# Kernel tuning notes

Hardware: AMD Instinct MI355X
Metric: run time of the kernel (lower is better)

Reference implementation:

```python
import jax, jax.numpy as jnp
import numpy as np

# token_type_vocab constants (closed over; original passes a dict)
WORD_TOKEN, SMILES_TOKEN, VALUE_TOKEN, CLS_TOKEN, SEP_TOKEN, MASK_TOKEN = 0, 1, 2, 3, 4, 5
FP_DIM, HID, COL_VOCAB, MAX_POS, TT_VOCAB = 768, 768, 1000, 512, 8
B, S = 64, 512


def setup_inputs() -> dict:
    key = jax.random.key(0)
    ks = jax.random.split(key, 16)
    scale = 0.02
    return {
        "batch_size": B,
        "max_batch_seq_len": S,
        "SMILES_fps": jax.random.normal(ks[0], (B, S, FP_DIM), jnp.float32),
        "word_tokens_ref": jax.random.randint(ks[1], (B, S), 0, COL_VOCAB),
        "values_ref": jax.random.normal(ks[2], (B, S), jnp.float32),
        "token_type_ids": jax.random.randint(ks[3], (B, S), 0, 6),
        "position_ids": jax.random.randint(ks[4], (B, S), 0, MAX_POS),
        "fc1_w": jax.random.normal(ks[5], (FP_DIM, 4 * FP_DIM), jnp.float32) * scale,
        "fc1_b": jnp.zeros((4 * FP_DIM,), jnp.float32),
        "fc2_w": jax.random.normal(ks[6], (4 * FP_DIM, HID), jnp.float32) * scale,
        "fc2_b": jnp.zeros((HID,), jnp.float32),
        "prop_emb": jax.random.normal(ks[7], (COL_VOCAB, HID), jnp.float32) * scale,
        "val_w": jax.random.normal(ks[8], (HID,), jnp.float32) * scale,  # Linear(1, HID) weight
        "val_b": jnp.zeros((HID,), jnp.float32),
        "pos_emb": jax.random.normal(ks[9], (MAX_POS, HID), jnp.float32) * scale,
        "type_emb": jax.random.normal(ks[10], (TT_VOCAB, HID), jnp.float32) * scale,
        "ln_g": jnp.ones((HID,), jnp.float32),
        "ln_b": jnp.zeros((HID,), jnp.float32),
    }


def reference(batch_size, max_batch_seq_len, SMILES_fps, word_tokens_ref, values_ref,
              token_type_ids, position_ids, fc1_w, fc1_b, fc2_w, fc2_b, prop_emb,
              val_w, val_b, pos_emb, type_emb, ln_g, ln_b):
    word_mask = token_type_ids == WORD_TOKEN
    smiles_mask = token_type_ids == SMILES_TOKEN
    value_mask = token_type_ids == VALUE_TOKEN
    # Faithful to source: '&' of mutually exclusive equalities -> always False
    special_mask = (token_type_ids == CLS_TOKEN) & (token_type_ids == SEP_TOKEN) & (token_type_ids == MASK_TOKEN)

    # branch embeddings computed densely, selected per token (masks are disjoint)
    word_e = prop_emb[word_tokens_ref]                                   # [B,S,H]
    smiles_e = jax.nn.relu(jnp.einsum('bsf,fd->bsd', SMILES_fps, fc1_w) + fc1_b)
    smiles_e = jnp.einsum('bsf,fd->bsd', smiles_e, fc2_w) + fc2_b        # [B,S,H]
    value_e = values_ref[..., None] * val_w + val_b                      # [B,S,H]
    special_e = type_emb[token_type_ids]                                 # [B,S,H]

    input_embeddings = jnp.zeros_like(word_e)
    input_embeddings = jnp.where(word_mask[..., None], word_e, input_embeddings)
    input_embeddings = jnp.where(smiles_mask[..., None], smiles_e, input_embeddings)
    input_embeddings = jnp.where(value_mask[..., None], value_e, input_embeddings)
    input_embeddings = jnp.where(special_mask[..., None], special_e, input_embeddings)

    emb = input_embeddings + pos_emb[position_ids] + type_emb[token_type_ids]
    mu = jnp.mean(emb, axis=-1, keepdims=True)
    var = jnp.mean(jnp.square(emb - mu), axis=-1, keepdims=True)
    emb = (emb - mu) * jax.lax.rsqrt(var + 1e-12) * ln_g + ln_b
    return emb  # dropout_rate=0 (eval): identity
```

## Files before the change

### kernel.cpp

```cpp
#include <hip/hip_runtime.h>
#include <hip/hip_bf16.h>
#include <stdint.h>


typedef __bf16 bf16x8 __attribute__((ext_vector_type(8)));
typedef float f32x4 __attribute__((ext_vector_type(4)));

__device__ __forceinline__ unsigned short f2bf(float f) {
  union { float f; unsigned int u; } c; c.f = f;
  unsigned int u = c.u;
  return (unsigned short)((u + 0x7FFFu + ((u >> 16) & 1u)) >> 16);
}
__device__ __forceinline__ float bf2f(unsigned short b) {
  union { unsigned int u; float f; } c; c.u = ((unsigned int)b) << 16;
  return c.f;
}
__device__ __forceinline__ void barrier_sync() {
  asm volatile("" ::: "memory");
  __builtin_amdgcn_sched_barrier(0);
  __builtin_amdgcn_s_barrier();
  __builtin_amdgcn_sched_barrier(0);
  asm volatile("" ::: "memory");
}

__global__ __launch_bounds__(256) void k_prep(
    const float* __restrict__ fc1_w, const float* __restrict__ fc2_w,
    unsigned short* __restrict__ w1t, unsigned short* __restrict__ w2t,
    int* __restrict__ counter) {
  if (blockIdx.x == 0 && threadIdx.x == 0) *counter = 0;
  __shared__ float tile[32][33];
  int b = blockIdx.x;
  const float* src;
  unsigned short* dst;
  int R, C, bx, by;
  if (b < 2304) {
    src = fc1_w; dst = w1t; R = 768; C = 3072;
    bx = (b % 96) * 32; by = (b / 96) * 32;
  } else {
    b -= 2304;
    src = fc2_w; dst = w2t; R = 3072; C = 768;
    bx = (b % 24) * 32; by = (b / 24) * 32;
  }
  int tx = threadIdx.x & 31;
  int ty = threadIdx.x >> 5;
#pragma unroll
  for (int i = 0; i < 4; i++) {
    int r = by + ty + i * 8;
    tile[ty + i * 8][tx] = src[(size_t)r * C + bx + tx];
  }
  __syncthreads();
#pragma unroll
  for (int i = 0; i < 4; i++) {
    int c = bx + ty + i * 8;
    dst[(size_t)c * R + by + tx] = f2bf(tile[tx][ty + i * 8]);
  }
}

__global__ void k_compact(const int* __restrict__ tt, int* __restrict__ counter,
                          int* __restrict__ idx, int* __restrict__ slot, int BS) {
  int t = blockIdx.x * 256 + threadIdx.x;
  if (t >= BS) return;
  if (tt[t] == 1) {
    int s = atomicAdd(counter, 1);
    idx[s] = t;
    slot[t] = s;
  }
}

__global__ __launch_bounds__(256) void k_gather(
    const float* __restrict__ fps, const int* __restrict__ idx,
    const int* __restrict__ counter, unsigned short* __restrict__ A1, int cap) {
  int wave = threadIdx.x >> 6, lane = threadIdx.x & 63;
  int s = blockIdx.x * 4 + wave;
  int n = *counter;
  int n_pad = (n + 127) & ~127;
  if (n_pad > cap) n_pad = cap;
  if (s >= n_pad) return;
  ushort4* dst = (ushort4*)(A1 + (size_t)s * 768);
  if (s < n) {
    const float4* srcr = (const float4*)(fps + (size_t)idx[s] * 768);
#pragma unroll
    for (int i = 0; i < 3; i++) {
      float4 v = srcr[lane + (i << 6)];
      ushort4 o;
      o.x = f2bf(v.x); o.y = f2bf(v.y); o.z = f2bf(v.z); o.w = f2bf(v.w);
      dst[lane + (i << 6)] = o;
    }
  } else {
    ushort4 z = {0, 0, 0, 0};
#pragma unroll
    for (int i = 0; i < 3; i++) dst[lane + (i << 6)] = z;
  }
}

template <int MODE, int NB, int KS, int AST, int BST>
__global__ __launch_bounds__(256) void k_gemm(
    const unsigned short* __restrict__ A,
    const unsigned short* __restrict__ BT,
    const float* __restrict__ bias,
    unsigned short* __restrict__ C,
    const int* __restrict__ counter, int N, int cap) {
  int n = *counter;
  int n_pad = (n + 127) & ~127;
  if (n_pad > cap) n_pad = cap;
  const int mb = n_pad >> 7;

  constexpr int NCOL = NB * KS;
  constexpr int C_CH = (KS > 1) ? ((KS == 4) ? 4 : 2) : 2;
  constexpr int A_CH = 8 / C_CH;
  constexpr int CLEN = NCOL / C_CH;
  constexpr int KSL = AST / KS;
  constexpr int KITER = KSL / 64;

  const int bid = blockIdx.x;
  const int xcd = bid & 7;
  const int j = bid >> 3;
  const int mc = xcd / C_CH, cc = xcd % C_CH;
  const int q = mb / A_CH, r = mb % A_CH;
  const int mlen = q + (mc < r ? 1 : 0);
  const int mbase = mc * q + (mc < r ? mc : r);
  if (j >= mlen * CLEN) return;
  const int m_blk = mbase + j / CLEN;
  const int c_blk = cc * CLEN + j % CLEN;
  const int ks = c_blk / NB;
  const int nb = c_blk % NB;
  const int m0 = m_blk * 128, n0 = nb * 128;
  const int k0g = ks * KSL;

  __shared__ __attribute__((aligned(128))) char smem[65536];
  auto lds = (__attribute__((address_space(3))) char*)smem;

  const int t = threadIdx.x;
  const int wave = t >> 6;
  const int lane = t & 63;
  const int wm = (wave >> 1) * 64;
  const int wn = (wave & 1) * 64;

  f32x4 acc[4][4] = {};

  auto stage = [&](int kt, int bufbase) {
#pragma unroll
    for (int i = 0; i < 4; i++) {
      int c = i * 256 + t;
      int rr = c >> 3;
      int k8 = ((c & 7) ^ (rr & 7)) << 3;
      const unsigned short* ga = A + (size_t)(m0 + rr) * AST + k0g + kt * 64 + k8;
      __builtin_amdgcn_global_load_lds(
          (const __attribute__((address_space(1))) void*)ga,
          (__attribute__((address_space(3))) void*)(lds + bufbase + i * 4096 + wave * 1024),
          16, 0, 0);
    }
#pragma unroll
    for (int i = 0; i < 4; i++) {
      int c = i * 256 + t;
      int rr = c >> 3;
      int k8 = ((c & 7) ^ (rr & 7)) << 3;
      const unsigned short* gb = BT + (size_t)(n0 + rr) * BST + k0g + kt * 64 + k8;
      __builtin_amdgcn_global_load_lds(
          (const __attribute__((address_space(1))) void*)gb,
          (__attribute__((address_space(3))) void*)(lds + bufbase + 16384 + i * 4096 + wave * 1024),
          16, 0, 0);
    }
  };

  stage(0, 0);
  for (int it = 0; it < KITER; ++it) {
    const int cur = it & 1, nxt = cur ^ 1;
    if (it + 1 < KITER) {
      stage(it + 1, nxt * 32768);
      __builtin_amdgcn_sched_barrier(0);
      asm volatile("s_waitcnt vmcnt(8)" ::: "memory");
    } else {
      asm volatile("s_waitcnt vmcnt(0)" ::: "memory");
    }
    barrier_sync();
    const int bufbase = cur * 32768;
#pragma unroll
    for (int kk = 0; kk < 2; kk++) {
      bf16x8 af[4], bfr[4];
      int kbyte = (kk * 32 + ((lane >> 4) * 8)) * 2;
#pragma unroll
      for (int mi = 0; mi < 4; mi++) {
        int rr = wm + mi * 16 + (lane & 15);
        af[mi] = *(const bf16x8*)(smem + bufbase + rr * 128 + (kbyte ^ ((rr & 7) << 4)));
      }
#pragma unroll
      for (int ni = 0; ni < 4; ni++) {
        int rr = wn + ni * 16 + (lane & 15);
        bfr[ni] = *(const bf16x8*)(smem + bufbase + 16384 + rr * 128 + (kbyte ^ ((rr & 7) << 4)));
      }
#pragma unroll
      for (int mi = 0; mi < 4; mi++)
#pragma unroll
        for (int ni = 0; ni < 4; ni++)
          acc[mi][ni] = __builtin_amdgcn_mfma_f32_16x16x32_bf16(
              af[mi], bfr[ni], acc[mi][ni], 0, 0, 0);
    }
    asm volatile("s_waitcnt lgkmcnt(0)" ::: "memory");
    barrier_sync();
  }

#pragma unroll
  for (int ni = 0; ni < 4; ni++) {
    int col = n0 + wn + ni * 16 + (lane & 15);
    float bv = (MODE == 1) ? bias[col] : 0.f;
#pragma unroll
    for (int mi = 0; mi < 4; mi++) {
#pragma unroll
      for (int j2 = 0; j2 < 4; j2++) {
        int row = m0 + wm + mi * 16 + ((lane >> 4) * 4) + j2;
        float v = acc[mi][ni][j2] + bv;
        if constexpr (MODE == 1) {
          v = v > 0.f ? v : 0.f;
          C[(size_t)row * N + col] = f2bf(v);
        } else {
          C[((size_t)ks * cap + row) * N + col] = f2bf(v);
        }
      }
    }
  }
}

__global__ __launch_bounds__(256) void k_assemble(
    const unsigned short* __restrict__ sout, const float* __restrict__ fc2b,
    const int* __restrict__ slot,
    const int* __restrict__ ttid, const int* __restrict__ word,
    const float* __restrict__ values, const int* __restrict__ posid,
    const float* __restrict__ prop, const float* __restrict__ valw,
    const float* __restrict__ valb, const float* __restrict__ pose,
    const float* __restrict__ tye, const float* __restrict__ lng,
    const float* __restrict__ lnb, float* __restrict__ out, int BS, int cap) {
  int wave = threadIdx.x >> 6, lane = threadIdx.x & 63;
  int t = blockIdx.x * 4 + wave;
  if (t >= BS) return;
  int tt = ttid[t];

  float v[12];
  if (tt == 1) {
    int sl = slot[t];
    const ushort4* pr[2];
#pragma unroll
    for (int p = 0; p < 2; p++)
      pr[p] = (const ushort4*)(sout + ((size_t)p * cap + sl) * 768);
    const float4* b4 = (const float4*)fc2b;
#pragma unroll
    for (int i = 0; i < 3; i++) {
      float4 b = b4[lane + (i << 6)];
      float a0 = b.x, a1 = b.y, a2 = b.z, a3 = b.w;
#pragma unroll
      for (int p = 0; p < 2; p++) {
        ushort4 u = pr[p][lane + (i << 6)];
        a0 += bf2f(u.x); a1 += bf2f(u.y); a2 += bf2f(u.z); a3 += bf2f(u.w);
      }
      v[4 * i] = a0; v[4 * i + 1] = a1; v[4 * i + 2] = a2; v[4 * i + 3] = a3;
    }
  } else if (tt == 0) {
    const float4* row = (const float4*)(prop + (size_t)word[t] * 768);
#pragma unroll
    for (int i = 0; i < 3; i++) {
      float4 x = row[lane + (i << 6)];
      v[4 * i] = x.x; v[4 * i + 1] = x.y; v[4 * i + 2] = x.z; v[4 * i + 3] = x.w;
    }
  } else if (tt == 2) {
    float val = values[t];
#pragma unroll
    for (int i = 0; i < 3; i++) {
      float4 w = ((const float4*)valw)[lane + (i << 6)];
      float4 b = ((const float4*)valb)[lane + (i << 6)];
      v[4 * i] = val * w.x + b.x; v[4 * i + 1] = val * w.y + b.y;
      v[4 * i + 2] = val * w.z + b.z; v[4 * i + 3] = val * w.w + b.w;
    }
  } else {
#pragma unroll
    for (int j = 0; j < 12; j++) v[j] = 0.f;
  }

  const float4* p4 = (const float4*)(pose + (size_t)posid[t] * 768);
  const float4* ty4 = (const float4*)(tye + (size_t)tt * 768);
#pragma unroll
  for (int i = 0; i < 3; i++) {
    float4 p = p4[lane + (i << 6)];
    float4 y = ty4[lane + (i << 6)];
    v[4 * i] += p.x + y.x; v[4 * i + 1] += p.y + y.y;
    v[4 * i + 2] += p.z + y.z; v[4 * i + 3] += p.w + y.w;
  }

  float s = 0.f;
#pragma unroll
  for (int j = 0; j < 12; j++) s += v[j];
#pragma unroll
  for (int o = 32; o >= 1; o >>= 1) s += __shfl_xor(s, o);
  float mu = s * (1.0f / 768.0f);

  float qv = 0.f;
#pragma unroll
  for (int j = 0; j < 12; j++) { float d = v[j] - mu; qv += d * d; }
#pragma unroll
  for (int o = 32; o >= 1; o >>= 1) qv += __shfl_xor(qv, o);
  float rs = 1.0f / sqrtf(qv * (1.0f / 768.0f) + 1e-12f);

  float4* o4 = (float4*)(out + (size_t)t * 768);
#pragma unroll
  for (int i = 0; i < 3; i++) {
    float4 g = ((const float4*)lng)[lane + (i << 6)];
    float4 b = ((const float4*)lnb)[lane + (i << 6)];
    float4 r;
    r.x = (v[4 * i] - mu) * rs * g.x + b.x;
    r.y = (v[4 * i + 1] - mu) * rs * g.y + b.y;
    r.z = (v[4 * i + 2] - mu) * rs * g.z + b.z;
    r.w = (v[4 * i + 3] - mu) * rs * g.w + b.w;
    o4[lane + (i << 6)] = r;
  }
}

extern "C" void kernel_launch(void* const* d_in, const int* in_sizes, int n_in,
                              void* d_out, int out_size, void* d_ws, size_t ws_size,
                              hipStream_t stream) {
  const int BS = in_sizes[3];
  const float* fps    = (const float*)d_in[2];
  const int*   word   = (const int*)d_in[3];
  const float* values = (const float*)d_in[4];
  const int*   tt     = (const int*)d_in[5];
  const int*   pos    = (const int*)d_in[6];
  const float* fc1_w  = (const float*)d_in[7];
  const float* fc1_b  = (const float*)d_in[8];
  const float* fc2_w  = (const float*)d_in[9];
  const float* fc2_b  = (const float*)d_in[10];
  const float* prop   = (const float*)d_in[11];
  const float* valw   = (const float*)d_in[12];
  const float* valb   = (const float*)d_in[13];
  const float* pose   = (const float*)d_in[14];
  const float* tye    = (const float*)d_in[15];
  const float* lng    = (const float*)d_in[16];
  const float* lnb    = (const float*)d_in[17];
  float* out = (float*)d_out;

  char* ws = (char*)d_ws;
  const size_t off_idx  = 256;
  const size_t off_slot = off_idx + (size_t)BS * 4;
  const size_t off_w1t  = off_slot + (size_t)BS * 4;
  const size_t off_w2t  = off_w1t + (size_t)768 * 3072 * 2;
  const size_t off_A1   = off_w2t + (size_t)3072 * 768 * 2;
  const size_t fixed    = off_A1;
  size_t avail = ws_size > fixed ? ws_size - fixed : 0;

  const size_t per_tok = 768 * 2 + 3072 * 2 + 2 * 768 * 2;
  int cap = 8192;
  if (avail < (size_t)8192 * per_tok) {
    long c = (long)(avail / per_tok);
    c &= ~127L;
    if (c < 128) c = 128;
    cap = (int)c;
  }
  const int MBcap = cap / 128;

  const size_t off_h1   = off_A1 + (size_t)cap * 768 * 2;
  const size_t off_sout = off_h1 + (size_t)cap * 3072 * 2;

  int* counter = (int*)(ws + 0);
  int* idx     = (int*)(ws + off_idx);
  int* slot    = (int*)(ws + off_slot);
  unsigned short* w1t = (unsigned short*)(ws + off_w1t);
  unsigned short* w2t = (unsigned short*)(ws + off_w2t);
  unsigned short* A1  = (unsigned short*)(ws + off_A1);
  unsigned short* h1  = (unsigned short*)(ws + off_h1);
  unsigned short* sout = (unsigned short*)(ws + off_sout);

  k_prep<<<4608, 256, 0, stream>>>(fc1_w, fc2_w, w1t, w2t, counter);
  k_compact<<<(BS + 255) / 256, 256, 0, stream>>>(tt, counter, idx, slot, BS);
  k_gather<<<cap / 4, 256, 0, stream>>>(fps, idx, counter, A1, cap);

  k_gemm<1, 24, 1, 768, 768><<<24 * MBcap, 256, 0, stream>>>(
      A1, w1t, fc1_b, h1, counter, 3072, cap);

  k_gemm<0, 6, 2, 3072, 3072><<<12 * MBcap, 256, 0, stream>>>(
      h1, w2t, nullptr, sout, counter, 768, cap);

  k_assemble<<<(BS + 3) / 4, 256, 0, stream>>>(
      sout, fc2_b, slot, tt, word, values, pos, prop, valw, valb, pose, tye,
      lng, lnb, out, BS, cap);
}
```

Baseline: 123.6 us.

## Halve GEMM K-tile to 32, raise occupancy, and split fc2 into four K slices

The GEMM's K step drops from 64 to 32, which halves LDS use to 32KB per block and gets a new swizzled layout that pairs rows. The launch bound now requests 5 waves per SIMD so more blocks can be resident. The second GEMM goes from 2 to 4 K splits and launches twice as many blocks, and the assemble kernel sums four partial bf16 outputs. In exchange there are twice as many barrier iterations per tile, extra partial-sum traffic and workspace, and more bf16 rounding in the partials.

New measurement: 140.0 us. 1.13x slower.

```diff
diff --git a/kernel.cpp b/kernel.cpp
--- a/kernel.cpp
+++ b/kernel.cpp
@@ -94,7 +94,7 @@
 }
 
 template <int MODE, int NB, int KS, int AST, int BST>
-__global__ __launch_bounds__(256) void k_gemm(
+__global__ __launch_bounds__(256, 5) void k_gemm(
     const unsigned short* __restrict__ A,
     const unsigned short* __restrict__ BT,
     const float* __restrict__ bias,
@@ -106,11 +106,11 @@
   const int mb = n_pad >> 7;
 
   constexpr int NCOL = NB * KS;
-  constexpr int C_CH = (KS > 1) ? ((KS == 4) ? 4 : 2) : 2;
+  constexpr int C_CH = (KS == 4) ? 4 : 2;
   constexpr int A_CH = 8 / C_CH;
   constexpr int CLEN = NCOL / C_CH;
   constexpr int KSL = AST / KS;
-  constexpr int KITER = KSL / 64;
+  constexpr int KITER = KSL / 32;
 
   const int bid = blockIdx.x;
   const int xcd = bid & 7;
@@ -127,7 +127,7 @@
   const int m0 = m_blk * 128, n0 = nb * 128;
   const int k0g = ks * KSL;
 
-  __shared__ __attribute__((aligned(128))) char smem[65536];
+  __shared__ __attribute__((aligned(128))) char smem[32768];
   auto lds = (__attribute__((address_space(3))) char*)smem;
 
   const int t = threadIdx.x;
@@ -140,25 +140,27 @@
 
   auto stage = [&](int kt, int bufbase) {
 #pragma unroll
-    for (int i = 0; i < 4; i++) {
-      int c = i * 256 + t;
-      int rr = c >> 3;
-      int k8 = ((c & 7) ^ (rr & 7)) << 3;
-      const unsigned short* ga = A + (size_t)(m0 + rr) * AST + k0g + kt * 64 + k8;
+    for (int i = 0; i < 2; i++) {
+      int l = i * 256 + t;
+      int L = l >> 3, p = l & 7;
+      int rr = 2 * L + (p >> 2);
+      int c = (p & 3) ^ (L & 3);
+      const unsigned short* ga = A + (size_t)(m0 + rr) * AST + k0g + kt * 32 + c * 8;
       __builtin_amdgcn_global_load_lds(
           (const __attribute__((address_space(1))) void*)ga,
           (__attribute__((address_space(3))) void*)(lds + bufbase + i * 4096 + wave * 1024),
           16, 0, 0);
     }
 #pragma unroll
-    for (int i = 0; i < 4; i++) {
-      int c = i * 256 + t;
-      int rr = c >> 3;
-      int k8 = ((c & 7) ^ (rr & 7)) << 3;
-      const unsigned short* gb = BT + (size_t)(n0 + rr) * BST + k0g + kt * 64 + k8;
+    for (int i = 0; i < 2; i++) {
+      int l = i * 256 + t;
+      int L = l >> 3, p = l & 7;
+      int rr = 2 * L + (p >> 2);
+      int c = (p & 3) ^ (L & 3);
+      const unsigned short* gb = BT + (size_t)(n0 + rr) * BST + k0g + kt * 32 + c * 8;
       __builtin_amdgcn_global_load_lds(
           (const __attribute__((address_space(1))) void*)gb,
-          (__attribute__((address_space(3))) void*)(lds + bufbase + 16384 + i * 4096 + wave * 1024),
+          (__attribute__((address_space(3))) void*)(lds + bufbase + 8192 + i * 4096 + wave * 1024),
           16, 0, 0);
     }
   };
@@ -167,27 +169,28 @@
   for (int it = 0; it < KITER; ++it) {
     const int cur = it & 1, nxt = cur ^ 1;
     if (it + 1 < KITER) {
-      stage(it + 1, nxt * 32768);
+      stage(it + 1, nxt * 16384);
       __builtin_amdgcn_sched_barrier(0);
-      asm volatile("s_waitcnt vmcnt(8)" ::: "memory");
+      asm volatile("s_waitcnt vmcnt(4)" ::: "memory");
     } else {
       asm volatile("s_waitcnt vmcnt(0)" ::: "memory");
     }
     barrier_sync();
-    const int bufbase = cur * 32768;
-#pragma unroll
-    for (int kk = 0; kk < 2; kk++) {
+    const int bufbase = cur * 16384;
+    {
       bf16x8 af[4], bfr[4];
-      int kbyte = (kk * 32 + ((lane >> 4) * 8)) * 2;
+      const int kc = lane >> 4;
 #pragma unroll
       for (int mi = 0; mi < 4; mi++) {
         int rr = wm + mi * 16 + (lane & 15);
-        af[mi] = *(const bf16x8*)(smem + bufbase + rr * 128 + (kbyte ^ ((rr & 7) << 4)));
+        int a16 = (rr >> 1) * 8 + ((rr & 1) << 2) + (kc ^ ((rr >> 1) & 3));
+        af[mi] = *(const bf16x8*)(smem + bufbase + a16 * 16);
       }
 #pragma unroll
       for (int ni = 0; ni < 4; ni++) {
         int rr = wn + ni * 16 + (lane & 15);
-        bfr[ni] = *(const bf16x8*)(smem + bufbase + 16384 + rr * 128 + (kbyte ^ ((rr & 7) << 4)));
+        int b16 = (rr >> 1) * 8 + ((rr & 1) << 2) + (kc ^ ((rr >> 1) & 3));
+        bfr[ni] = *(const bf16x8*)(smem + bufbase + 8192 + b16 * 16);
       }
 #pragma unroll
       for (int mi = 0; mi < 4; mi++)
@@ -238,9 +241,9 @@
   float v[12];
   if (tt == 1) {
     int sl = slot[t];
-    const ushort4* pr[2];
-#pragma unroll
-    for (int p = 0; p < 2; p++)
+    const ushort4* pr[4];
+#pragma unroll
+    for (int p = 0; p < 4; p++)
       pr[p] = (const ushort4*)(sout + ((size_t)p * cap + sl) * 768);
     const float4* b4 = (const float4*)fc2b;
 #pragma unroll
@@ -248,7 +251,7 @@
       float4 b = b4[lane + (i << 6)];
       float a0 = b.x, a1 = b.y, a2 = b.z, a3 = b.w;
 #pragma unroll
-      for (int p = 0; p < 2; p++) {
+      for (int p = 0; p < 4; p++) {
         ushort4 u = pr[p][lane + (i << 6)];
         a0 += bf2f(u.x); a1 += bf2f(u.y); a2 += bf2f(u.z); a3 += bf2f(u.w);
       }
@@ -344,10 +347,10 @@
   const size_t fixed    = off_A1;
   size_t avail = ws_size > fixed ? ws_size - fixed : 0;
 
-  const size_t per_tok = 768 * 2 + 3072 * 2 + 2 * 768 * 2;
+  const size_t per_tok4 = 768 * 2 + 3072 * 2 + 4 * 768 * 2;
   int cap = 8192;
-  if (avail < (size_t)8192 * per_tok) {
-    long c = (long)(avail / per_tok);
+  if (avail < (size_t)8192 * per_tok4) {
+    long c = (long)(avail / per_tok4);
     c &= ~127L;
     if (c < 128) c = 128;
     cap = (int)c;
@@ -373,7 +376,7 @@
   k_gemm<1, 24, 1, 768, 768><<<24 * MBcap, 256, 0, stream>>>(
       A1, w1t, fc1_b, h1, counter, 3072, cap);
 
-  k_gemm<0, 6, 2, 3072, 3072><<<12 * MBcap, 256, 0, stream>>>(
+  k_gemm<0, 6, 4, 3072, 3072><<<24 * MBcap, 256, 0, stream>>>(
       h1, w2t, nullptr, sout, counter, 768, cap);
 
   k_assemble<<<(BS + 3) / 4, 256, 0, stream>>>(
```
